# Optimization experiments

Measured on AMD Instinct MI355X. Metric: run time of the kernel, lower is better.

Reference implementation:

```python
import jax, jax.numpy as jnp
import numpy as np

N = 100000      # nodes
E = 1600000     # edges (avg degree 16)
D_IN, D_H1, D_H2, D_OUT = 512, 256, 256, 64


def setup_inputs() -> dict:
    key = jax.random.key(0)
    ks = jax.random.split(key, 8)
    x = jax.random.normal(ks[0], (N, D_IN), dtype=jnp.float32)
    row = jax.random.randint(ks[1], (E,), 0, N, dtype=jnp.int32)
    col = jax.random.randint(ks[2], (E,), 0, N, dtype=jnp.int32)
    vals = jax.random.uniform(ks[3], (E,), dtype=jnp.float32)
    # xavier-normal-ish scaling for weights
    W1 = jax.random.normal(ks[4], (D_IN, D_H1), dtype=jnp.float32) * np.sqrt(2.0 / (D_IN + D_H1))
    W2 = jax.random.normal(ks[5], (D_H1, D_H2), dtype=jnp.float32) * np.sqrt(2.0 / (D_H1 + D_H2))
    W3 = jax.random.normal(ks[6], (D_H2, D_OUT), dtype=jnp.float32) * np.sqrt(2.0 / (D_H2 + D_OUT))
    b1 = jnp.zeros((D_H1,), dtype=jnp.float32)
    b2 = jnp.zeros((D_H2,), dtype=jnp.float32)
    b3 = jnp.zeros((D_OUT,), dtype=jnp.float32)
    return {"x": x, "row": row, "col": col, "vals": vals,
            "W1": W1, "b1": b1, "W2": W2, "b2": b2, "W3": W3, "b3": b3}


def reference(x, row, col, vals, W1, b1, W2, b2, W3, b3):
    n = x.shape[0]

    def spmm(h):
        # out[i] = sum_{e: row[e]==i} vals[e] * h[col[e]]  (COO spmm)
        return jax.ops.segment_sum(vals[:, None] * h[col], row, num_segments=n)

    # layer 1: linear -> spmm -> relu  (dropout p=0 -> identity)
    h = jax.nn.relu(spmm(x @ W1 + b1))
    # layer 2
    h = jax.nn.relu(spmm(h @ W2 + b2))
    # output layer: no activation, no dropout
    return spmm(h @ W3 + b3)
```

## Files before the change

kernel.cpp:

```cpp
#include <hip/hip_runtime.h>

typedef _Float16 f16;
typedef _Float16 f16x4 __attribute__((ext_vector_type(4)));
typedef _Float16 f16x8 __attribute__((ext_vector_type(8)));
typedef float f32x4 __attribute__((ext_vector_type(4)));

#define DEVI __device__ __forceinline__

static constexpr int CAP = 64;

DEVI void g2l16(const void* g, void* l) {
  __builtin_amdgcn_global_load_lds(
      (const __attribute__((address_space(1))) void*)g,
      (__attribute__((address_space(3))) void*)l, 16, 0, 0);
}

DEVI f16x8 cvt8(float4 a, float4 b) {
  f16x8 r;
  r[0] = (f16)a.x; r[1] = (f16)a.y; r[2] = (f16)a.z; r[3] = (f16)a.w;
  r[4] = (f16)b.x; r[5] = (f16)b.y; r[6] = (f16)b.z; r[7] = (f16)b.w;
  return r;
}

__global__ __launch_bounds__(256)
void prep_w(const float* __restrict__ W1, const float* __restrict__ W2,
            const float* __restrict__ W3, f16* __restrict__ WT1,
            f16* __restrict__ WT2, f16* __restrict__ WT3) {
  int t = blockIdx.x * 256 + threadIdx.x;
  if (t < 131072) {
    int n = t >> 9, k = t & 511;
    WT1[t] = (f16)W1[k * 256 + n];
  } else if (t < 131072 + 65536) {
    int u = t - 131072; int n = u >> 8, k = u & 255;
    WT2[u] = (f16)W2[k * 256 + n];
  } else if (t < 131072 + 65536 + 16384) {
    int u = t - 131072 - 65536; int n = u >> 8, k = u & 255;
    WT3[u] = (f16)W3[k * 64 + n];
  }
}

__global__ __launch_bounds__(256)
void build_slots(const int* __restrict__ row, const int* __restrict__ col,
                 const float* __restrict__ vals, int* __restrict__ cnt,
                 int2* __restrict__ slots, int E) {
  int e = blockIdx.x * 256 + threadIdx.x;
  if (e >= E) return;
  int r = row[e];
  int p = atomicAdd(&cnt[r], 1);
  if (p < CAP) slots[(size_t)r * CAP + p] = make_int2(col[e], __float_as_int(vals[e]));
}

template <int BN, bool AF32>
__global__ __launch_bounds__(256)
void gemm_kern(const void* __restrict__ Ap, const f16* __restrict__ WT,
               const float* __restrict__ bias, f16* __restrict__ C,
               int M, int K, int N) {
  constexpr int BM = 128;
  constexpr int NT = BN / 32;
  __shared__ f16 As[BM * 32];
  __shared__ f16 Bs[BN * 32];

  const int tid = threadIdx.x;
  const int wave = tid >> 6, lane = tid & 63;
  const int wm = wave >> 1, wn = wave & 1;
  const int quad = lane >> 4, l16 = lane & 15;
  const int bm = blockIdx.x, bn = blockIdx.y;
  const int r0 = bm * BM;

  f32x4 acc[4][NT];
#pragma unroll
  for (int mt = 0; mt < 4; ++mt)
#pragma unroll
    for (int nt = 0; nt < NT; ++nt) {
      f32x4 z = {0.f, 0.f, 0.f, 0.f};
      acc[mt][nt] = z;
    }

  const int kiters = K >> 5;
  for (int kb = 0; kb < kiters; ++kb) {
    if constexpr (AF32) {
      const float* Af = (const float*)Ap;
      int row = r0 + (tid >> 1);
      row = min(row, M - 1);
      const int half = tid & 1;
      const float4* gp = (const float4*)(Af + (size_t)row * K + kb * 32 + half * 16);
      float4 v0 = gp[0], v1 = gp[1], v2 = gp[2], v3 = gp[3];
      f16x8* dst = (f16x8*)&As[(tid >> 1) * 32 + half * 16];
      dst[0] = cvt8(v0, v1);
      dst[1] = cvt8(v2, v3);
    } else {
      const f16* Ah = (const f16*)Ap;
#pragma unroll
      for (int t = 0; t < 2; ++t) {
        int inst = wave * 2 + t;
        int row = r0 + inst * 16 + (lane >> 2);
        row = min(row, M - 1);
        const f16* gp = Ah + (size_t)row * K + kb * 32 + (lane & 3) * 8;
        g2l16(gp, &As[inst * 16 * 32]);
      }
    }
#pragma unroll
    for (int t = 0; t < BN / 64; ++t) {
      int inst = wave * (BN / 64) + t;
      int n = bn * BN + inst * 16 + (lane >> 2);
      const f16* gp = WT + (size_t)n * K + kb * 32 + (lane & 3) * 8;
      g2l16(gp, &Bs[inst * 16 * 32]);
    }
    __syncthreads();

    f16x8 af[4], bf[NT];
#pragma unroll
    for (int mt = 0; mt < 4; ++mt)
      af[mt] = *(const f16x8*)&As[(wm * 64 + mt * 16 + l16) * 32 + quad * 8];
#pragma unroll
    for (int nt = 0; nt < NT; ++nt)
      bf[nt] = *(const f16x8*)&Bs[(wn * (BN / 2) + nt * 16 + l16) * 32 + quad * 8];
#pragma unroll
    for (int mt = 0; mt < 4; ++mt)
#pragma unroll
      for (int nt = 0; nt < NT; ++nt)
        acc[mt][nt] = __builtin_amdgcn_mfma_f32_16x16x32_f16(af[mt], bf[nt], acc[mt][nt], 0, 0, 0);
    __syncthreads();
  }

  float bv[NT];
#pragma unroll
  for (int nt = 0; nt < NT; ++nt)
    bv[nt] = bias[bn * BN + wn * (BN / 2) + nt * 16 + l16];
#pragma unroll
  for (int mt = 0; mt < 4; ++mt) {
#pragma unroll
    for (int nt = 0; nt < NT; ++nt) {
      int colg = bn * BN + wn * (BN / 2) + nt * 16 + l16;
#pragma unroll
      for (int r = 0; r < 4; ++r) {
        int grow = r0 + wm * 64 + mt * 16 + quad * 4 + r;
        if (grow < M)
          C[(size_t)grow * N + colg] = (f16)(acc[mt][nt][r] + bv[nt]);
      }
    }
  }
}

__global__ __launch_bounds__(256)
void spmm_relu256(const f16* __restrict__ T, const int2* __restrict__ slots,
                  const int* __restrict__ cnt, f16* __restrict__ H, int nrows) {
  const int wave = threadIdx.x >> 6, lane = threadIdx.x & 63;
  const int i = blockIdx.x * 4 + wave;
  if (i >= nrows) return;
  const int c = min(cnt[i], CAP);
  const int2* sl = slots + (size_t)i * CAP;
  float a0 = 0.f, a1 = 0.f, a2 = 0.f, a3 = 0.f;
  int j = 0;
  for (; j + 4 <= c; j += 4) {
    int2 e0 = sl[j], e1 = sl[j + 1], e2 = sl[j + 2], e3 = sl[j + 3];
    f16x4 u0 = ((const f16x4*)(T + (size_t)e0.x * 256))[lane];
    f16x4 u1 = ((const f16x4*)(T + (size_t)e1.x * 256))[lane];
    f16x4 u2 = ((const f16x4*)(T + (size_t)e2.x * 256))[lane];
    f16x4 u3 = ((const f16x4*)(T + (size_t)e3.x * 256))[lane];
    float v0 = __int_as_float(e0.y), v1 = __int_as_float(e1.y);
    float v2 = __int_as_float(e2.y), v3 = __int_as_float(e3.y);
    a0 += v0 * (float)u0.x + v1 * (float)u1.x + v2 * (float)u2.x + v3 * (float)u3.x;
    a1 += v0 * (float)u0.y + v1 * (float)u1.y + v2 * (float)u2.y + v3 * (float)u3.y;
    a2 += v0 * (float)u0.z + v1 * (float)u1.z + v2 * (float)u2.z + v3 * (float)u3.z;
    a3 += v0 * (float)u0.w + v1 * (float)u1.w + v2 * (float)u2.w + v3 * (float)u3.w;
  }
  for (; j < c; ++j) {
    int2 e = sl[j];
    f16x4 u = ((const f16x4*)(T + (size_t)e.x * 256))[lane];
    float v = __int_as_float(e.y);
    a0 += v * (float)u.x; a1 += v * (float)u.y;
    a2 += v * (float)u.z; a3 += v * (float)u.w;
  }
  f16x4 o;
  o.x = (f16)fmaxf(a0, 0.f); o.y = (f16)fmaxf(a1, 0.f);
  o.z = (f16)fmaxf(a2, 0.f); o.w = (f16)fmaxf(a3, 0.f);
  ((f16x4*)(H + (size_t)i * 256))[lane] = o;
}

__global__ __launch_bounds__(256)
void spmm_out64(const f16* __restrict__ T, const int2* __restrict__ slots,
                const int* __restrict__ cnt, float* __restrict__ out, int nrows) {
  const int wave = threadIdx.x >> 6, lane = threadIdx.x & 63;
  const int i = blockIdx.x * 4 + wave;
  if (i >= nrows) return;
  const int c = min(cnt[i], CAP);
  const int2* sl = slots + (size_t)i * CAP;
  float a = 0.f;
  int j = 0;
  for (; j + 4 <= c; j += 4) {
    int2 e0 = sl[j], e1 = sl[j + 1], e2 = sl[j + 2], e3 = sl[j + 3];
    float u0 = (float)T[(size_t)e0.x * 64 + lane];
    float u1 = (float)T[(size_t)e1.x * 64 + lane];
    float u2 = (float)T[(size_t)e2.x * 64 + lane];
    float u3 = (float)T[(size_t)e3.x * 64 + lane];
    a += __int_as_float(e0.y) * u0 + __int_as_float(e1.y) * u1
       + __int_as_float(e2.y) * u2 + __int_as_float(e3.y) * u3;
  }
  for (; j < c; ++j) {
    int2 e = sl[j];
    a += __int_as_float(e.y) * (float)T[(size_t)e.x * 64 + lane];
  }
  out[(size_t)i * 64 + lane] = a;
}

extern "C" void kernel_launch(void* const* d_in, const int* in_sizes, int n_in,
                              void* d_out, int out_size, void* d_ws, size_t ws_size,
                              hipStream_t stream) {
  const float* x    = (const float*)d_in[0];
  const int*   row  = (const int*)d_in[1];
  const int*   col  = (const int*)d_in[2];
  const float* vals = (const float*)d_in[3];
  const float* W1   = (const float*)d_in[4];
  const float* b1   = (const float*)d_in[5];
  const float* W2   = (const float*)d_in[6];
  const float* b2   = (const float*)d_in[7];
  const float* W3   = (const float*)d_in[8];
  const float* b3   = (const float*)d_in[9];
  float* out = (float*)d_out;

  const int N = in_sizes[0] / 512;
  const int E = in_sizes[1];

  char* ws = (char*)d_ws;
  const size_t MiB = 1ull << 20;
  int*  cnt   = (int*)ws;
  int2* slots = (int2*)(ws + 1 * MiB);
  f16*  WT1   = (f16*)(ws + 52 * MiB);
  f16*  WT2   = WT1 + 256 * 512;
  f16*  WT3   = WT2 + 256 * 256;
  f16*  T     = (f16*)(ws + 53 * MiB);
  f16*  H     = (f16*)(ws + 104 * MiB);

  hipMemsetAsync(cnt, 0, (size_t)N * sizeof(int), stream);
  prep_w<<<(131072 + 65536 + 16384 + 255) / 256, 256, 0, stream>>>(W1, W2, W3, WT1, WT2, WT3);
  build_slots<<<(E + 255) / 256, 256, 0, stream>>>(row, col, vals, cnt, slots, E);

  dim3 g12((N + 127) / 128, 2);
  dim3 g3((N + 127) / 128, 1);
  dim3 gs((N + 3) / 4);

  gemm_kern<128, true><<<g12, 256, 0, stream>>>(x, WT1, b1, T, N, 512, 256);
  spmm_relu256<<<gs, 256, 0, stream>>>(T, slots, cnt, H, N);
  gemm_kern<128, false><<<g12, 256, 0, stream>>>(H, WT2, b2, T, N, 256, 256);
  spmm_relu256<<<gs, 256, 0, stream>>>(T, slots, cnt, H, N);
  gemm_kern<64, false><<<g3, 256, 0, stream>>>(H, WT3, b3, T, N, 256, 64);
  spmm_out64<<<gs, 256, 0, stream>>>(T, slots, cnt, out, N);
}
```

Baseline: 829.5 us.

## Replace LDS-tiled GEMM with direct-load MFMA GEMM and widen SpMM gathers

The GEMM drops its shared-memory staging and barriers. Each wave now loads A and B fragments straight from global memory into registers, with a fixed K per template and a launch bound of three blocks per unit. Each wave covers all N columns, either split in half across wave pairs or taken whole, so A is read once per block. The SpMM kernels split the wave into halves or quarters that gather different neighbor rows with wider vector loads, then combine the partial sums with cross-lane shuffles. The aim is to cut sync overhead and raise bytes per gather load, at the cost of more redundant global and L2 reads of the weights.

```diff
diff --git a/kernel.cpp b/kernel.cpp
--- a/kernel.cpp
+++ b/kernel.cpp
@@ -8,12 +8,6 @@
 #define DEVI __device__ __forceinline__
 
 static constexpr int CAP = 64;
-
-DEVI void g2l16(const void* g, void* l) {
-  __builtin_amdgcn_global_load_lds(
-      (const __attribute__((address_space(1))) void*)g,
-      (__attribute__((address_space(3))) void*)l, 16, 0, 0);
-}
 
 DEVI f16x8 cvt8(float4 a, float4 b) {
   f16x8 r;
@@ -50,91 +44,73 @@
   if (p < CAP) slots[(size_t)r * CAP + p] = make_int2(col[e], __float_as_int(vals[e]));
 }
 
-template <int BN, bool AF32>
-__global__ __launch_bounds__(256)
-void gemm_kern(const void* __restrict__ Ap, const f16* __restrict__ WT,
-               const float* __restrict__ bias, f16* __restrict__ C,
-               int M, int K, int N) {
-  constexpr int BM = 128;
-  constexpr int NT = BN / 32;
-  __shared__ f16 As[BM * 32];
-  __shared__ f16 Bs[BN * 32];
-
+template <int NT, int WN, int KI, bool AF32>
+__global__ __launch_bounds__(256, 3)
+void gemm_direct(const void* __restrict__ Ap, const f16* __restrict__ WT,
+                 const float* __restrict__ bias, f16* __restrict__ C,
+                 int M, int N) {
+  constexpr int K = KI * 32;
   const int tid = threadIdx.x;
   const int wave = tid >> 6, lane = tid & 63;
-  const int wm = wave >> 1, wn = wave & 1;
   const int quad = lane >> 4, l16 = lane & 15;
-  const int bm = blockIdx.x, bn = blockIdx.y;
-  const int r0 = bm * BM;
-
-  f32x4 acc[4][NT];
-#pragma unroll
-  for (int mt = 0; mt < 4; ++mt)
+  const int wn = (WN == 1) ? 0 : (wave & 1);
+  const int wm = (WN == 1) ? wave : (wave >> 1);
+  constexpr int RPB = (4 / WN) * 32;
+  const int r0 = blockIdx.x * RPB + wm * 32;
+  const int n0 = wn * (NT * 16);
+
+  f32x4 acc[2][NT];
+#pragma unroll
+  for (int mt = 0; mt < 2; ++mt)
 #pragma unroll
     for (int nt = 0; nt < NT; ++nt) {
       f32x4 z = {0.f, 0.f, 0.f, 0.f};
       acc[mt][nt] = z;
     }
 
-  const int kiters = K >> 5;
-  for (int kb = 0; kb < kiters; ++kb) {
+  const int ar0 = min(r0 + l16, M - 1);
+  const int ar1 = min(r0 + 16 + l16, M - 1);
+
+#pragma unroll 2
+  for (int kb = 0; kb < KI; ++kb) {
+    const int k0 = kb * 32 + quad * 8;
+    f16x8 af[2];
     if constexpr (AF32) {
       const float* Af = (const float*)Ap;
-      int row = r0 + (tid >> 1);
-      row = min(row, M - 1);
-      const int half = tid & 1;
-      const float4* gp = (const float4*)(Af + (size_t)row * K + kb * 32 + half * 16);
-      float4 v0 = gp[0], v1 = gp[1], v2 = gp[2], v3 = gp[3];
-      f16x8* dst = (f16x8*)&As[(tid >> 1) * 32 + half * 16];
-      dst[0] = cvt8(v0, v1);
-      dst[1] = cvt8(v2, v3);
+      const float4* p0 = (const float4*)(Af + (size_t)ar0 * K + k0);
+      const float4* p1 = (const float4*)(Af + (size_t)ar1 * K + k0);
+      float4 u0 = p0[0], u1 = p0[1];
+      float4 v0 = p1[0], v1 = p1[1];
+      af[0] = cvt8(u0, u1);
+      af[1] = cvt8(v0, v1);
     } else {
       const f16* Ah = (const f16*)Ap;
-#pragma unroll
-      for (int t = 0; t < 2; ++t) {
-        int inst = wave * 2 + t;
-        int row = r0 + inst * 16 + (lane >> 2);
-        row = min(row, M - 1);
-        const f16* gp = Ah + (size_t)row * K + kb * 32 + (lane & 3) * 8;
-        g2l16(gp, &As[inst * 16 * 32]);
-      }
+      af[0] = *(const f16x8*)(Ah + (size_t)ar0 * K + k0);
+      af[1] = *(const f16x8*)(Ah + (size_t)ar1 * K + k0);
     }
-#pragma unroll
-    for (int t = 0; t < BN / 64; ++t) {
-      int inst = wave * (BN / 64) + t;
-      int n = bn * BN + inst * 16 + (lane >> 2);
-      const f16* gp = WT + (size_t)n * K + kb * 32 + (lane & 3) * 8;
-      g2l16(gp, &Bs[inst * 16 * 32]);
-    }
-    __syncthreads();
-
-    f16x8 af[4], bf[NT];
-#pragma unroll
-    for (int mt = 0; mt < 4; ++mt)
-      af[mt] = *(const f16x8*)&As[(wm * 64 + mt * 16 + l16) * 32 + quad * 8];
+    f16x8 bf[NT];
 #pragma unroll
     for (int nt = 0; nt < NT; ++nt)
-      bf[nt] = *(const f16x8*)&Bs[(wn * (BN / 2) + nt * 16 + l16) * 32 + quad * 8];
-#pragma unroll
-    for (int mt = 0; mt < 4; ++mt)
+      bf[nt] = *(const f16x8*)(WT + (size_t)(n0 + nt * 16 + l16) * K + k0);
+#pragma unroll
+    for (int mt = 0; mt < 2; ++mt)
 #pragma unroll
       for (int nt = 0; nt < NT; ++nt)
         acc[mt][nt] = __builtin_amdgcn_mfma_f32_16x16x32_f16(af[mt], bf[nt], acc[mt][nt], 0, 0, 0);
-    __syncthreads();
   }
 
   float bv[NT];
 #pragma unroll
   for (int nt = 0; nt < NT; ++nt)
-    bv[nt] = bias[bn * BN + wn * (BN / 2) + nt * 16 + l16];
-#pragma unroll
-  for (int mt = 0; mt < 4; ++mt) {
+    bv[nt] = bias[n0 + nt * 16 + l16];
+#pragma unroll
+  for (int mt = 0; mt < 2; ++mt) {
 #pragma unroll
     for (int nt = 0; nt < NT; ++nt) {
-      int colg = bn * BN + wn * (BN / 2) + nt * 16 + l16;
+      const int colg = n0 + nt * 16 + l16;
 #pragma unroll
       for (int r = 0; r < 4; ++r) {
-        int grow = r0 + wm * 64 + mt * 16 + quad * 4 + r;
+        int grow = r0 + mt * 16 + quad * 4 + r;
         if (grow < M)
           C[(size_t)grow * N + colg] = (f16)(acc[mt][nt][r] + bv[nt]);
       }
@@ -150,32 +126,42 @@
   if (i >= nrows) return;
   const int c = min(cnt[i], CAP);
   const int2* sl = slots + (size_t)i * CAP;
-  float a0 = 0.f, a1 = 0.f, a2 = 0.f, a3 = 0.f;
+  const int half = lane >> 5, fl = lane & 31;
+
+  float a[8];
+#pragma unroll
+  for (int k = 0; k < 8; ++k) a[k] = 0.f;
+
   int j = 0;
-  for (; j + 4 <= c; j += 4) {
-    int2 e0 = sl[j], e1 = sl[j + 1], e2 = sl[j + 2], e3 = sl[j + 3];
-    f16x4 u0 = ((const f16x4*)(T + (size_t)e0.x * 256))[lane];
-    f16x4 u1 = ((const f16x4*)(T + (size_t)e1.x * 256))[lane];
-    f16x4 u2 = ((const f16x4*)(T + (size_t)e2.x * 256))[lane];
-    f16x4 u3 = ((const f16x4*)(T + (size_t)e3.x * 256))[lane];
+  for (; j + 8 <= c; j += 8) {
+    int2 e0 = sl[j + half], e1 = sl[j + 2 + half];
+    int2 e2 = sl[j + 4 + half], e3 = sl[j + 6 + half];
+    f16x8 u0 = *(const f16x8*)(T + (size_t)e0.x * 256 + fl * 8);
+    f16x8 u1 = *(const f16x8*)(T + (size_t)e1.x * 256 + fl * 8);
+    f16x8 u2 = *(const f16x8*)(T + (size_t)e2.x * 256 + fl * 8);
+    f16x8 u3 = *(const f16x8*)(T + (size_t)e3.x * 256 + fl * 8);
     float v0 = __int_as_float(e0.y), v1 = __int_as_float(e1.y);
     float v2 = __int_as_float(e2.y), v3 = __int_as_float(e3.y);
-    a0 += v0 * (float)u0.x + v1 * (float)u1.x + v2 * (float)u2.x + v3 * (float)u3.x;
-    a1 += v0 * (float)u0.y + v1 * (float)u1.y + v2 * (float)u2.y + v3 * (float)u3.y;
-    a2 += v0 * (float)u0.z + v1 * (float)u1.z + v2 * (float)u2.z + v3 * (float)u3.z;
-    a3 += v0 * (float)u0.w + v1 * (float)u1.w + v2 * (float)u2.w + v3 * (float)u3.w;
-  }
-  for (; j < c; ++j) {
-    int2 e = sl[j];
-    f16x4 u = ((const f16x4*)(T + (size_t)e.x * 256))[lane];
-    float v = __int_as_float(e.y);
-    a0 += v * (float)u.x; a1 += v * (float)u.y;
-    a2 += v * (float)u.z; a3 += v * (float)u.w;
-  }
-  f16x4 o;
-  o.x = (f16)fmaxf(a0, 0.f); o.y = (f16)fmaxf(a1, 0.f);
-  o.z = (f16)fmaxf(a2, 0.f); o.w = (f16)fmaxf(a3, 0.f);
-  ((f16x4*)(H + (size_t)i * 256))[lane] = o;
+#pragma unroll
+    for (int k = 0; k < 8; ++k)
+      a[k] += v0 * (float)u0[k] + v1 * (float)u1[k] + v2 * (float)u2[k] + v3 * (float)u3[k];
+  }
+  for (; j < c; j += 2) {
+    int jj = j + half;
+    int2 e = sl[min(jj, c - 1)];
+    float v = (jj < c) ? __int_as_float(e.y) : 0.f;
+    f16x8 u = *(const f16x8*)(T + (size_t)e.x * 256 + fl * 8);
+#pragma unroll
+    for (int k = 0; k < 8; ++k) a[k] += v * (float)u[k];
+  }
+#pragma unroll
+  for (int k = 0; k < 8; ++k) a[k] += __shfl_xor(a[k], 32, 64);
+  if (half == 0) {
+    f16x8 o;
+#pragma unroll
+    for (int k = 0; k < 8; ++k) o[k] = (f16)fmaxf(a[k], 0.f);
+    *(f16x8*)(H + (size_t)i * 256 + fl * 8) = o;
+  }
 }
 
 __global__ __launch_bounds__(256)
@@ -186,22 +172,38 @@
   if (i >= nrows) return;
   const int c = min(cnt[i], CAP);
   const int2* sl = slots + (size_t)i * CAP;
-  float a = 0.f;
+  const int sub = lane >> 4, fl = lane & 15;
+
+  float a[4];
+#pragma unroll
+  for (int k = 0; k < 4; ++k) a[k] = 0.f;
+
   int j = 0;
-  for (; j + 4 <= c; j += 4) {
-    int2 e0 = sl[j], e1 = sl[j + 1], e2 = sl[j + 2], e3 = sl[j + 3];
-    float u0 = (float)T[(size_t)e0.x * 64 + lane];
-    float u1 = (float)T[(size_t)e1.x * 64 + lane];
-    float u2 = (float)T[(size_t)e2.x * 64 + lane];
-    float u3 = (float)T[(size_t)e3.x * 64 + lane];
-    a += __int_as_float(e0.y) * u0 + __int_as_float(e1.y) * u1
-       + __int_as_float(e2.y) * u2 + __int_as_float(e3.y) * u3;
-  }
-  for (; j < c; ++j) {
-    int2 e = sl[j];
-    a += __int_as_float(e.y) * (float)T[(size_t)e.x * 64 + lane];
-  }
-  out[(size_t)i * 64 + lane] = a;
+  for (; j + 8 <= c; j += 8) {
+    int2 e0 = sl[j + sub], e1 = sl[j + 4 + sub];
+    f16x4 u0 = *(const f16x4*)(T + (size_t)e0.x * 64 + fl * 4);
+    f16x4 u1 = *(const f16x4*)(T + (size_t)e1.x * 64 + fl * 4);
+    float v0 = __int_as_float(e0.y), v1 = __int_as_float(e1.y);
+#pragma unroll
+    for (int k = 0; k < 4; ++k) a[k] += v0 * (float)u0[k] + v1 * (float)u1[k];
+  }
+  for (; j < c; j += 4) {
+    int jj = j + sub;
+    int2 e = sl[min(jj, c - 1)];
+    float v = (jj < c) ? __int_as_float(e.y) : 0.f;
+    f16x4 u = *(const f16x4*)(T + (size_t)e.x * 64 + fl * 4);
+#pragma unroll
+    for (int k = 0; k < 4; ++k) a[k] += v * (float)u[k];
+  }
+#pragma unroll
+  for (int k = 0; k < 4; ++k) {
+    a[k] += __shfl_xor(a[k], 16, 64);
+    a[k] += __shfl_xor(a[k], 32, 64);
+  }
+  if (sub == 0) {
+    float4 o = make_float4(a[0], a[1], a[2], a[3]);
+    *(float4*)(out + (size_t)i * 64 + fl * 4) = o;
+  }
 }
 
 extern "C" void kernel_launch(void* const* d_in, const int* in_sizes, int n_in,
@@ -236,14 +238,14 @@
   prep_w<<<(131072 + 65536 + 16384 + 255) / 256, 256, 0, stream>>>(W1, W2, W3, WT1, WT2, WT3);
   build_slots<<<(E + 255) / 256, 256, 0, stream>>>(row, col, vals, cnt, slots, E);
 
-  dim3 g12((N + 127) / 128, 2);
-  dim3 g3((N + 127) / 128, 1);
-  dim3 gs((N + 3) / 4);
-
-  gemm_kern<128, true><<<g12, 256, 0, stream>>>(x, WT1, b1, T, N, 512, 256);
+  const int g12 = (N + 63) / 64;
+  const int g3  = (N + 127) / 128;
+  const int gs  = (N + 3) / 4;
+
+  gemm_direct<8, 2, 16, true><<<g12, 256, 0, stream>>>(x, WT1, b1, T, N, 256);
   spmm_relu256<<<gs, 256, 0, stream>>>(T, slots, cnt, H, N);
-  gemm_kern<128, false><<<g12, 256, 0, stream>>>(H, WT2, b2, T, N, 256, 256);
+  gemm_direct<8, 2, 8, false><<<g12, 256, 0, stream>>>(H, WT2, b2, T, N, 256);
   spmm_relu256<<<gs, 256, 0, stream>>>(T, slots, cnt, H, N);
-  gemm_kern<64, false><<<g3, 256, 0, stream>>>(H, WT3, b3, T, N, 256, 64);
+  gemm_direct<4, 1, 8, false><<<g3, 256, 0, stream>>>(H, WT3, b3, T, N, 64);
   spmm_out64<<<gs, 256, 0, stream>>>(T, slots, cnt, out, N);
 }
```

Result: slower. 907.8 us (+9.4%).
